# Optimization experiments

Hardware: AMD Instinct MI355X
Metric: run time of the kernel (lower is better)

Reference implementation:

```python
import jax, jax.numpy as jnp
import numpy as np

N_NODES = 100000
IN_CH = 128
HID = 128   # 2 * out_channels
OUT = 64
N_EDGES = 1600000


def gcn_conv(x, W, b, src, dst, n_nodes):
    """PyG GCNConv: add self-loops, symmetric normalization D^-1/2 (A+I) D^-1/2 X W + b."""
    h = x @ W  # [N, F_out]
    ones = jnp.ones(dst.shape[0], dtype=h.dtype)
    # degree of target nodes, +1 for self loop
    deg = jax.ops.segment_sum(ones, dst, num_segments=n_nodes) + 1.0
    dinv = jnp.where(deg > 0, jax.lax.rsqrt(deg), 0.0)  # [N]
    norm = dinv[src] * dinv[dst]  # [E]
    agg = jax.ops.segment_sum(h[src] * norm[:, None], dst, num_segments=n_nodes)
    # self-loop contribution: norm_ii = dinv_i^2 (avoids materializing extra edges)
    agg = agg + h * (dinv * dinv)[:, None]
    return agg + b


def setup_inputs() -> dict:
    key = jax.random.key(0)
    ks = jax.random.split(key, 8)
    x = jax.random.normal(ks[0], (N_NODES, IN_CH), dtype=jnp.float32)
    edge_index = jax.random.randint(ks[1], (2, N_EDGES), 0, N_NODES, dtype=jnp.int64)
    # Glorot-style params
    W1 = jax.random.normal(ks[2], (IN_CH, HID), dtype=jnp.float32) / np.sqrt(IN_CH)
    b1 = jnp.zeros((HID,), dtype=jnp.float32)
    W_mu = jax.random.normal(ks[3], (HID, OUT), dtype=jnp.float32) / np.sqrt(HID)
    b_mu = jnp.zeros((OUT,), dtype=jnp.float32)
    W_ls = jax.random.normal(ks[4], (HID, OUT), dtype=jnp.float32) / np.sqrt(HID)
    b_ls = jnp.zeros((OUT,), dtype=jnp.float32)
    return {"x": x, "edge_index": edge_index, "W1": W1, "b1": b1,
            "W_mu": W_mu, "b_mu": b_mu, "W_ls": W_ls, "b_ls": b_ls}


def reference(x, edge_index, W1, b1, W_mu, b_mu, W_ls, b_ls):
    src, dst = edge_index[0], edge_index[1]
    n = x.shape[0]
    h = jax.nn.relu(gcn_conv(x, W1, b1, src, dst, n))
    mu = gcn_conv(h, W_mu, b_mu, src, dst, n)
    logstd = gcn_conv(h, W_ls, b_ls, src, dst, n)
    return (mu, logstd)
```

## Files before the change

kernel.cpp:

```cpp
#include <hip/hip_runtime.h>
#include <hip/hip_bf16.h>
#include <hip/hip_fp16.h>
#include <stdint.h>

#define N_NODES 100000
#define IN_CH   128
#define HID     128
#define OUT_CH  64
#define N_EDGES 1600000

#define NB    196
#define NBLK  250
#define EPB   6400

typedef __attribute__((ext_vector_type(8))) short  s16x8;
typedef __attribute__((ext_vector_type(4))) float  f32x4;

__device__ __forceinline__ __half2 as_h2(unsigned int u) { return *(__half2*)&u; }


__global__ __launch_bounds__(256) void k_phaseA(const int* __restrict__ dst,
                                                int* __restrict__ Cm) {
    __shared__ int hist[NB];
    int blk = blockIdx.x, t = threadIdx.x;
    if (t < NB) hist[t] = 0;
    __syncthreads();
    int base = blk * EPB;
#pragma unroll 5
    for (int k = 0; k < EPB / 256; k++) {
        int d = dst[base + k * 256 + t];
        atomicAdd(&hist[d >> 9], 1);
    }
    __syncthreads();
    if (t < NB) Cm[blk * NB + t] = hist[t];
}

__global__ __launch_bounds__(256) void k_scanBkt(int* __restrict__ Cm,
                                                 int* __restrict__ bktSum) {
    __shared__ int sdata[256];
    int b = blockIdx.x, t = threadIdx.x;
    int v = (t < NBLK) ? Cm[t * NB + b] : 0;
    sdata[t] = v;
    __syncthreads();
    int val = v;
    for (int off = 1; off < 256; off <<= 1) {
        int tmp = (t >= off) ? sdata[t - off] : 0;
        __syncthreads();
        val += tmp;
        sdata[t] = val;
        __syncthreads();
    }
    if (t < NBLK) Cm[t * NB + b] = val - v;
    if (t == 255) bktSum[b] = val;
}

__global__ __launch_bounds__(256) void k_scanBase(const int* __restrict__ bktSum,
                                                  int* __restrict__ bktBase) {
    __shared__ int sdata[256];
    int t = threadIdx.x;
    int v = (t < NB) ? bktSum[t] : 0;
    sdata[t] = v;
    __syncthreads();
    int val = v;
    for (int off = 1; off < 256; off <<= 1) {
        int tmp = (t >= off) ? sdata[t - off] : 0;
        __syncthreads();
        val += tmp;
        sdata[t] = val;
        __syncthreads();
    }
    if (t < NB) bktBase[t] = val - v;
    if (t == 0) bktBase[NB] = N_EDGES;
}

__global__ __launch_bounds__(256) void k_phaseB(const int* __restrict__ src,
                                                const int* __restrict__ dst,
                                                const int* __restrict__ Cm,
                                                const int* __restrict__ bktBase,
                                                unsigned int* __restrict__ bucketed) {
    __shared__ int offs[NB];
    int blk = blockIdx.x, t = threadIdx.x;
    if (t < NB) offs[t] = Cm[blk * NB + t] + bktBase[t];
    __syncthreads();
    int base = blk * EPB;
#pragma unroll 5
    for (int k = 0; k < EPB / 256; k++) {
        int e = base + k * 256 + t;
        int d = dst[e];
        int sv = src[e];
        int pos = atomicAdd(&offs[d >> 9], 1);
        bucketed[pos] = ((unsigned int)sv << 9) | (unsigned int)(d & 511);
    }
}

__global__ __launch_bounds__(512) void k_phaseC(const unsigned int* __restrict__ bucketed,
                                                const int* __restrict__ bktBase,
                                                int* __restrict__ rowptr,
                                                float* __restrict__ dinvg,
                                                unsigned int* __restrict__ dinvh2,
                                                int* __restrict__ csr_src) {
    __shared__ int cnt[512];
    __shared__ int cur[512];
    __shared__ int sdata[512];
    int b = blockIdx.x, t = threadIdx.x;
    int base = bktBase[b], endR = bktBase[b + 1];
    int nodeBase = b << 9;
    int nNodes = N_NODES - nodeBase;
    if (nNodes > 512) nNodes = 512;

    cnt[t] = 0;
    __syncthreads();
    for (int e = base + t; e < endR; e += 512)
        atomicAdd(&cnt[bucketed[e] & 511], 1);
    __syncthreads();

    int s = cnt[t];
    sdata[t] = s;
    __syncthreads();
    int val = s;
    for (int off = 1; off < 512; off <<= 1) {
        int tmp = (t >= off) ? sdata[t - off] : 0;
        __syncthreads();
        val += tmp;
        sdata[t] = val;
        __syncthreads();
    }
    cur[t] = val - s;
    if (t < nNodes) {
        rowptr[nodeBase + t] = base + val - s;
        float dv = rsqrtf((float)s + 1.0f);
        dinvg[nodeBase + t] = dv;
        __half hd = __float2half(dv);
        unsigned int hu = *(unsigned short*)&hd;
        dinvh2[nodeBase + t] = hu | (hu << 16);
    }
    if (b == NB - 1 && t == 0) rowptr[N_NODES] = N_EDGES;
    __syncthreads();

    for (int e = base + t; e < endR; e += 512) {
        unsigned int u = bucketed[e];
        int pos = base + atomicAdd(&cur[u & 511], 1);
        csr_src[pos] = (int)(u >> 9);
    }
}


__global__ __launch_bounds__(256) void k_prepW(const float* __restrict__ W1,
                                               const float* __restrict__ Wmu,
                                               const float* __restrict__ Wls,
                                               unsigned short* __restrict__ Wt1,
                                               unsigned short* __restrict__ WtC) {
    int idx = blockIdx.x * 256 + threadIdx.x;
    int n = idx >> 7, k = idx & 127;
    __half a = __float2half(W1[k * 128 + n]);
    __half b = __float2half((n < 64) ? Wmu[k * 64 + n] : Wls[k * 64 + (n - 64)]);
    Wt1[idx] = *(unsigned short*)&a;
    WtC[idx] = *(unsigned short*)&b;
}


#define LDA 136

__device__ __forceinline__ void gemm_core(const unsigned short* sA,
                                          const unsigned short* __restrict__ Wt,
                                          unsigned short* __restrict__ Y,
                                          int R0, int t) {
    int wv = t >> 6, l = t & 63;
    int quad = l >> 4, lm = l & 15;

    s16x8 a[2][4];
#pragma unroll
    for (int mt = 0; mt < 2; mt++)
#pragma unroll
        for (int ks = 0; ks < 4; ks++)
            a[mt][ks] = *(const s16x8*)(sA + (wv * 32 + mt * 16 + lm) * LDA +
                                        ks * 32 + quad * 8);

    f32x4 acc[2][8] = {};
#pragma unroll
    for (int nt = 0; nt < 8; nt++) {
        s16x8 b[4];
        const unsigned short* Wp = Wt + (nt * 16 + lm) * 128 + quad * 8;
#pragma unroll
        for (int ks = 0; ks < 4; ks++)
            b[ks] = *(const s16x8*)(Wp + ks * 32);
#pragma unroll
        for (int mt = 0; mt < 2; mt++) {
            f32x4 c = acc[mt][nt];
#pragma unroll
            for (int ks = 0; ks < 4; ks++)
                c = __builtin_amdgcn_mfma_f32_16x16x32_f16(a[mt][ks], b[ks], c, 0, 0, 0);
            acc[mt][nt] = c;
        }
    }

    int rbase = R0 + wv * 32 + quad * 4;
#pragma unroll
    for (int mt = 0; mt < 2; mt++)
#pragma unroll
        for (int nt = 0; nt < 8; nt++)
#pragma unroll
            for (int reg = 0; reg < 4; reg++) {
                int r = rbase + mt * 16 + reg;
                if (r < N_NODES) {
                    __half hv = __float2half(acc[mt][nt][reg]);
                    Y[(size_t)r * 128 + nt * 16 + lm] = *(unsigned short*)&hv;
                }
            }
}

__global__ __launch_bounds__(256) void k_gemm1(const float* __restrict__ X,
                                               const unsigned short* __restrict__ Wt,
                                               unsigned short* __restrict__ Y) {
    __shared__ unsigned short sA[128 * LDA];
    int t = threadIdx.x;
    int R0 = blockIdx.x * 128;
    int row = t >> 1, colb = (t & 1) * 64;
    bool valid = (R0 + row) < N_NODES;
    const float* Xr = X + (size_t)(R0 + row) * 128 + colb;
    unsigned short* dp = sA + row * LDA + colb;
#pragma unroll
    for (int j = 0; j < 16; j++) {
        float4 v = valid ? *(const float4*)(Xr + j * 4) : make_float4(0.f, 0.f, 0.f, 0.f);
        __half2 p0 = __floats2half2_rn(v.x, v.y);
        __half2 p1 = __floats2half2_rn(v.z, v.w);
        uint2 o;
        o.x = *(unsigned int*)&p0;
        o.y = *(unsigned int*)&p1;
        *(uint2*)(dp + j * 4) = o;
    }
    __syncthreads();
    gemm_core(sA, Wt, Y, R0, t);
}

__global__ __launch_bounds__(256) void k_gemm2(const unsigned short* __restrict__ Xh,
                                               const unsigned short* __restrict__ Wt,
                                               unsigned short* __restrict__ Y) {
    __shared__ unsigned short sA[128 * LDA];
    int t = threadIdx.x;
    int R0 = blockIdx.x * 128;
    int row = t >> 1, colb = (t & 1) * 64;
    bool valid = (R0 + row) < N_NODES;
    const unsigned short* Xr = Xh + (size_t)(R0 + row) * 128 + colb;
    unsigned short* dp = sA + row * LDA + colb;
#pragma unroll
    for (int j = 0; j < 8; j++) {
        uint4 v = valid ? *(const uint4*)(Xr + j * 8) : make_uint4(0u, 0u, 0u, 0u);
        *(uint4*)(dp + j * 8) = v;
    }
    __syncthreads();
    gemm_core(sA, Wt, Y, R0, t);
}


__device__ __forceinline__ float2 agg_gather(const unsigned short* __restrict__ tbl,
                                             const int* __restrict__ rowptr,
                                             const int* __restrict__ csr_src,
                                             const unsigned int* __restrict__ dh2,
                                             const float* __restrict__ dinv,
                                             int i, int c2, float* di_out) {
    float di = dinv[i];
    *di_out = di;
    unsigned int sv = *(const unsigned int*)(tbl + (size_t)i * 128 + c2);
    __half2 acc = __floats2half2_rn(0.f, 0.f);
    int beg = rowptr[i], end = rowptr[i + 1];
    for (int p = beg; p < end; p += 8) {
        int s[8]; unsigned int nv[8]; unsigned int r[8];
#pragma unroll
        for (int j = 0; j < 8; j++) {
            int q = p + j;
            s[j] = csr_src[q < end ? q : end - 1];
        }
#pragma unroll
        for (int j = 0; j < 8; j++) nv[j] = dh2[s[j]];
#pragma unroll
        for (int j = 0; j < 8; j++)
            r[j] = *(const unsigned int*)(tbl + (size_t)s[j] * 128 + c2);
#pragma unroll
        for (int j = 0; j < 8; j++) {
            unsigned int nn = (p + j < end) ? nv[j] : 0u;
            acc = __hfma2(as_h2(r[j]), as_h2(nn), acc);
        }
    }
    float2 f = __half22float2(acc);
    float2 hs = __half22float2(as_h2(sv));
    f.x = di * f.x + di * di * hs.x;
    f.y = di * f.y + di * di * hs.y;
    return f;
}

__global__ __launch_bounds__(256) void k_agg1(const unsigned short* __restrict__ h0,
                                              const int* __restrict__ rowptr,
                                              const int* __restrict__ csr_src,
                                              const unsigned int* __restrict__ dh2,
                                              const float* __restrict__ dinv,
                                              const float* __restrict__ b1,
                                              unsigned short* __restrict__ hb) {
    int lane = threadIdx.x & 63;
    int i = __builtin_amdgcn_readfirstlane(blockIdx.x * 4 + (threadIdx.x >> 6));
    int c2 = lane * 2;
    float di;
    float2 f = agg_gather(h0, rowptr, csr_src, dh2, dinv, i, c2, &di);
    f.x += b1[c2];
    f.y += b1[c2 + 1];
    f.x = f.x > 0.f ? f.x : 0.f;
    f.y = f.y > 0.f ? f.y : 0.f;
    __half2 o = __floats2half2_rn(f.x, f.y);
    *(unsigned int*)(hb + (size_t)i * 128 + c2) = *(unsigned int*)&o;
}

__global__ __launch_bounds__(256) void k_agg2(const unsigned short* __restrict__ tt,
                                              const int* __restrict__ rowptr,
                                              const int* __restrict__ csr_src,
                                              const unsigned int* __restrict__ dh2,
                                              const float* __restrict__ dinv,
                                              const float* __restrict__ bmu,
                                              const float* __restrict__ bls,
                                              float* __restrict__ out) {
    int lane = threadIdx.x & 63;
    int i = __builtin_amdgcn_readfirstlane(blockIdx.x * 4 + (threadIdx.x >> 6));
    int c2 = lane * 2;
    float di;
    float2 f = agg_gather(tt, rowptr, csr_src, dh2, dinv, i, c2, &di);
    if (lane < 32) {
        int c = c2;
        *(float2*)(out + (size_t)i * 64 + c) =
            make_float2(f.x + bmu[c], f.y + bmu[c + 1]);
    } else {
        int c = c2 - 64;
        *(float2*)(out + (size_t)N_NODES * 64 + (size_t)i * 64 + c) =
            make_float2(f.x + bls[c], f.y + bls[c + 1]);
    }
}


extern "C" void kernel_launch(void* const* d_in, const int* in_sizes, int n_in,
                              void* d_out, int out_size, void* d_ws, size_t ws_size,
                              hipStream_t stream) {
    const float* x    = (const float*)d_in[0];
    const int*   ei   = (const int*)d_in[1];
    const float* W1   = (const float*)d_in[2];
    const float* b1   = (const float*)d_in[3];
    const float* Wmu  = (const float*)d_in[4];
    const float* bmu  = (const float*)d_in[5];
    const float* Wls  = (const float*)d_in[6];
    const float* bls  = (const float*)d_in[7];
    const int* src = ei;
    const int* dst = ei + N_EDGES;

    char* p = (char*)d_ws;
    unsigned short* bufA = (unsigned short*)p; p += (size_t)N_NODES * 128 * 2;
    unsigned short* bufH = (unsigned short*)p; p += (size_t)N_NODES * 128 * 2;
    unsigned short* Wt1  = (unsigned short*)p; p += 128 * 128 * 2;
    unsigned short* WtC  = (unsigned short*)p; p += 128 * 128 * 2;
    int*   Cm      = (int*)p;   p += (size_t)NBLK * NB * 4;
    int*   bktSum  = (int*)p;   p += 256 * 4;
    int*   bktBase = (int*)p;   p += 256 * 4;
    int*   rowptr  = (int*)p;   p += 400016;
    float* dinv    = (float*)p; p += 400000;
    unsigned int* dinvh2 = (unsigned int*)p; p += 400000;
    unsigned int* bucketed = (unsigned int*)p; p += (size_t)N_EDGES * 4;
    int*   csr_src = (int*)p;   p += (size_t)N_EDGES * 4;

    k_phaseA<<<NBLK, 256, 0, stream>>>(dst, Cm);
    k_scanBkt<<<NB, 256, 0, stream>>>(Cm, bktSum);
    k_scanBase<<<1, 256, 0, stream>>>(bktSum, bktBase);
    k_phaseB<<<NBLK, 256, 0, stream>>>(src, dst, Cm, bktBase, bucketed);
    k_phaseC<<<NB, 512, 0, stream>>>(bucketed, bktBase, rowptr, dinv, dinvh2, csr_src);

    k_prepW<<<64, 256, 0, stream>>>(W1, Wmu, Wls, Wt1, WtC);

    int gblk = (N_NODES + 127) / 128;

    k_gemm1<<<gblk, 256, 0, stream>>>(x, Wt1, bufA);
    k_agg1<<<N_NODES / 4, 256, 0, stream>>>(bufA, rowptr, csr_src, dinvh2, dinv, b1, bufH);

    k_gemm2<<<gblk, 256, 0, stream>>>(bufH, WtC, bufA);
    k_agg2<<<N_NODES / 4, 256, 0, stream>>>(bufA, rowptr, csr_src, dinvh2, dinv,
                                            bmu, bls, (float*)d_out);
}
```

Before: 350.6 us.

## Store feature tables in 16-column slices and gather per slice across edges

The GEMM outputs and the hidden activations move from row-major [N,128] half to eight column slices of [N,16], each slice a contiguous array. Each aggregation block now handles one slice for four nodes. Within a wavefront, 8 lane groups each take a different edge and each lane loads 4 bytes of the slice, and the partial sums are combined with cross-lane shuffles. This keeps every gathered slice table small (about 3.2 MB) so it can stay resident in cache and improve hit rates on the random gathers. The cost is eight times more blocks, each re-reading the CSR indices and normalisation factors once per slice, plus extra shuffle reductions.

```diff
diff --git a/kernel.cpp b/kernel.cpp
--- a/kernel.cpp
+++ b/kernel.cpp
@@ -12,6 +12,8 @@
 #define NB    196
 #define NBLK  250
 #define EPB   6400
+
+#define SS    ((size_t)N_NODES * 16)
 
 typedef __attribute__((ext_vector_type(8))) short  s16x8;
 typedef __attribute__((ext_vector_type(4))) float  f32x4;
@@ -204,7 +206,7 @@
                 int r = rbase + mt * 16 + reg;
                 if (r < N_NODES) {
                     __half hv = __float2half(acc[mt][nt][reg]);
-                    Y[(size_t)r * 128 + nt * 16 + lm] = *(unsigned short*)&hv;
+                    Y[(size_t)nt * SS + (size_t)r * 16 + lm] = *(unsigned short*)&hv;
                 }
             }
 }
@@ -233,54 +235,59 @@
     gemm_core(sA, Wt, Y, R0, t);
 }
 
-__global__ __launch_bounds__(256) void k_gemm2(const unsigned short* __restrict__ Xh,
+__global__ __launch_bounds__(256) void k_gemm2(const unsigned short* __restrict__ Xs,
                                                const unsigned short* __restrict__ Wt,
                                                unsigned short* __restrict__ Y) {
     __shared__ unsigned short sA[128 * LDA];
     int t = threadIdx.x;
     int R0 = blockIdx.x * 128;
-    int row = t >> 1, colb = (t & 1) * 64;
-    bool valid = (R0 + row) < N_NODES;
-    const unsigned short* Xr = Xh + (size_t)(R0 + row) * 128 + colb;
-    unsigned short* dp = sA + row * LDA + colb;
-#pragma unroll
-    for (int j = 0; j < 8; j++) {
-        uint4 v = valid ? *(const uint4*)(Xr + j * 8) : make_uint4(0u, 0u, 0u, 0u);
-        *(uint4*)(dp + j * 8) = v;
+    int q = t >> 5;
+    int sub = t & 31;
+    int part = (sub & 1) * 8;
+#pragma unroll
+    for (int rr = 0; rr < 8; rr++) {
+        int row = rr * 16 + (sub >> 1);
+        int gr = R0 + row;
+        uint4 v = (gr < N_NODES)
+                      ? *(const uint4*)(Xs + (size_t)q * SS + (size_t)gr * 16 + part)
+                      : make_uint4(0u, 0u, 0u, 0u);
+        *(uint4*)(sA + row * LDA + q * 16 + part) = v;
     }
     __syncthreads();
     gemm_core(sA, Wt, Y, R0, t);
 }
 
 
-__device__ __forceinline__ float2 agg_gather(const unsigned short* __restrict__ tbl,
-                                             const int* __restrict__ rowptr,
-                                             const int* __restrict__ csr_src,
-                                             const unsigned int* __restrict__ dh2,
-                                             const float* __restrict__ dinv,
-                                             int i, int c2, float* di_out) {
+__device__ __forceinline__ float2 agg_gather_sl(const unsigned short* __restrict__ tb,
+                                                const int* __restrict__ rowptr,
+                                                const int* __restrict__ csr_src,
+                                                const unsigned int* __restrict__ dh2,
+                                                const float* __restrict__ dinv,
+                                                int i, int l) {
+    int g = l >> 3;
+    int cl = l & 7;
     float di = dinv[i];
-    *di_out = di;
-    unsigned int sv = *(const unsigned int*)(tbl + (size_t)i * 128 + c2);
+    unsigned int sv = *(const unsigned int*)(tb + (size_t)i * 16 + cl * 2);
     __half2 acc = __floats2half2_rn(0.f, 0.f);
     int beg = rowptr[i], end = rowptr[i + 1];
-    for (int p = beg; p < end; p += 8) {
-        int s[8]; unsigned int nv[8]; unsigned int r[8];
-#pragma unroll
-        for (int j = 0; j < 8; j++) {
-            int q = p + j;
-            s[j] = csr_src[q < end ? q : end - 1];
-        }
-#pragma unroll
-        for (int j = 0; j < 8; j++) nv[j] = dh2[s[j]];
-#pragma unroll
-        for (int j = 0; j < 8; j++)
-            r[j] = *(const unsigned int*)(tbl + (size_t)s[j] * 128 + c2);
-#pragma unroll
-        for (int j = 0; j < 8; j++) {
-            unsigned int nn = (p + j < end) ? nv[j] : 0u;
-            acc = __hfma2(as_h2(r[j]), as_h2(nn), acc);
-        }
+    for (int p = beg; p < end; p += 16) {
+        int q0 = p + g, q1 = p + 8 + g;
+        int s0 = __builtin_nontemporal_load(csr_src + (q0 < end ? q0 : end - 1));
+        int s1 = __builtin_nontemporal_load(csr_src + (q1 < end ? q1 : end - 1));
+        unsigned int n0 = dh2[s0];
+        unsigned int n1 = dh2[s1];
+        unsigned int r0 = *(const unsigned int*)(tb + (size_t)s0 * 16 + cl * 2);
+        unsigned int r1 = *(const unsigned int*)(tb + (size_t)s1 * 16 + cl * 2);
+        n0 = (q0 < end) ? n0 : 0u;
+        n1 = (q1 < end) ? n1 : 0u;
+        acc = __hfma2(as_h2(r0), as_h2(n0), acc);
+        acc = __hfma2(as_h2(r1), as_h2(n1), acc);
+    }
+#pragma unroll
+    for (int m = 8; m <= 32; m <<= 1) {
+        int v = *(int*)&acc;
+        int u = __shfl_xor(v, m);
+        acc = __hadd2(acc, *(__half2*)&u);
     }
     float2 f = __half22float2(acc);
     float2 hs = __half22float2(as_h2(sv));
@@ -296,17 +303,22 @@
                                               const float* __restrict__ dinv,
                                               const float* __restrict__ b1,
                                               unsigned short* __restrict__ hb) {
-    int lane = threadIdx.x & 63;
-    int i = __builtin_amdgcn_readfirstlane(blockIdx.x * 4 + (threadIdx.x >> 6));
-    int c2 = lane * 2;
-    float di;
-    float2 f = agg_gather(h0, rowptr, csr_src, dh2, dinv, i, c2, &di);
-    f.x += b1[c2];
-    f.y += b1[c2 + 1];
-    f.x = f.x > 0.f ? f.x : 0.f;
-    f.y = f.y > 0.f ? f.y : 0.f;
-    __half2 o = __floats2half2_rn(f.x, f.y);
-    *(unsigned int*)(hb + (size_t)i * 128 + c2) = *(unsigned int*)&o;
+    int l = threadIdx.x & 63;
+    int wv = threadIdx.x >> 6;
+    int slice = blockIdx.x & 7;
+    int i = __builtin_amdgcn_readfirstlane((blockIdx.x >> 3) * 4 + wv);
+    const unsigned short* tb = h0 + (size_t)slice * SS;
+    float2 f = agg_gather_sl(tb, rowptr, csr_src, dh2, dinv, i, l);
+    if (l < 8) {
+        int c = slice * 16 + l * 2;
+        f.x += b1[c];
+        f.y += b1[c + 1];
+        f.x = f.x > 0.f ? f.x : 0.f;
+        f.y = f.y > 0.f ? f.y : 0.f;
+        __half2 o = __floats2half2_rn(f.x, f.y);
+        *(unsigned int*)(hb + (size_t)slice * SS + (size_t)i * 16 + l * 2) =
+            *(unsigned int*)&o;
+    }
 }
 
 __global__ __launch_bounds__(256) void k_agg2(const unsigned short* __restrict__ tt,
@@ -317,19 +329,20 @@
                                               const float* __restrict__ bmu,
                                               const float* __restrict__ bls,
                                               float* __restrict__ out) {
-    int lane = threadIdx.x & 63;
-    int i = __builtin_amdgcn_readfirstlane(blockIdx.x * 4 + (threadIdx.x >> 6));
-    int c2 = lane * 2;
-    float di;
-    float2 f = agg_gather(tt, rowptr, csr_src, dh2, dinv, i, c2, &di);
-    if (lane < 32) {
-        int c = c2;
-        *(float2*)(out + (size_t)i * 64 + c) =
-            make_float2(f.x + bmu[c], f.y + bmu[c + 1]);
-    } else {
-        int c = c2 - 64;
-        *(float2*)(out + (size_t)N_NODES * 64 + (size_t)i * 64 + c) =
-            make_float2(f.x + bls[c], f.y + bls[c + 1]);
+    int l = threadIdx.x & 63;
+    int wv = threadIdx.x >> 6;
+    int slice = blockIdx.x & 7;
+    int i = __builtin_amdgcn_readfirstlane((blockIdx.x >> 3) * 4 + wv);
+    const unsigned short* tb = tt + (size_t)slice * SS;
+    float2 f = agg_gather_sl(tb, rowptr, csr_src, dh2, dinv, i, l);
+    if (l < 8) {
+        int c = slice * 16 + l * 2;
+        if (c < 64)
+            *(float2*)(out + (size_t)i * 64 + c) =
+                make_float2(f.x + bmu[c], f.y + bmu[c + 1]);
+        else
+            *(float2*)(out + (size_t)N_NODES * 64 + (size_t)i * 64 + (c - 64)) =
+                make_float2(f.x + bls[c - 64], f.y + bls[c - 63]);
     }
 }
 
@@ -371,11 +384,12 @@
     k_prepW<<<64, 256, 0, stream>>>(W1, Wmu, Wls, Wt1, WtC);
 
     int gblk = (N_NODES + 127) / 128;
+    int ablk = (N_NODES / 4) * 8;
 
     k_gemm1<<<gblk, 256, 0, stream>>>(x, Wt1, bufA);
-    k_agg1<<<N_NODES / 4, 256, 0, stream>>>(bufA, rowptr, csr_src, dinvh2, dinv, b1, bufH);
+    k_agg1<<<ablk, 256, 0, stream>>>(bufA, rowptr, csr_src, dinvh2, dinv, b1, bufH);
 
     k_gemm2<<<gblk, 256, 0, stream>>>(bufH, WtC, bufA);
-    k_agg2<<<N_NODES / 4, 256, 0, stream>>>(bufA, rowptr, csr_src, dinvh2, dinv,
-                                            bmu, bls, (float*)d_out);
-}
+    k_agg2<<<ablk, 256, 0, stream>>>(bufA, rowptr, csr_src, dinvh2, dinv,
+                                     bmu, bls, (float*)d_out);
+}
```

New measurement: 702.1 us. 2x slower.

## Fuse CSR build phases and weight prep into one cooperative kernel

Applied to the files above, without the earlier changes.

Merges the histogram, two scans, bucket scatter, per-bucket CSR finalize and weight transpose into one cooperative kernel that uses grid.sync between phases. This removes five kernel launches and their inter-kernel gaps. Bucket totals are now gathered with global atomics after a memset, and every block recomputes the base scan redundantly. Phase C runs with 256 threads handling two nodes each instead of 512, which lowers the parallelism of that stage.

```diff
diff --git a/kernel.cpp b/kernel.cpp
--- a/kernel.cpp
+++ b/kernel.cpp
@@ -1,7 +1,10 @@
 #include <hip/hip_runtime.h>
+#include <hip/hip_cooperative_groups.h>
 #include <hip/hip_bf16.h>
 #include <hip/hip_fp16.h>
 #include <stdint.h>
+
+namespace cg = cooperative_groups;
 
 #define N_NODES 100000
 #define IN_CH   128
@@ -10,7 +13,7 @@
 #define N_EDGES 1600000
 
 #define NB    196
-#define NBLK  250
+#define CSRG  250
 #define EPB   6400
 
 typedef __attribute__((ext_vector_type(8))) short  s16x8;
@@ -19,70 +22,85 @@
 __device__ __forceinline__ __half2 as_h2(unsigned int u) { return *(__half2*)&u; }
 
 
-__global__ __launch_bounds__(256) void k_phaseA(const int* __restrict__ dst,
-                                                int* __restrict__ Cm) {
+__global__ __launch_bounds__(256) void k_csr(
+    const float* __restrict__ W1, const float* __restrict__ Wmu,
+    const float* __restrict__ Wls,
+    unsigned short* __restrict__ Wt1, unsigned short* __restrict__ WtC,
+    const int* __restrict__ src, const int* __restrict__ dst,
+    int* __restrict__ Cm, int* __restrict__ bktSum,
+    unsigned int* __restrict__ bucketed,
+    int* __restrict__ rowptr, float* __restrict__ dinvg,
+    unsigned int* __restrict__ dinvh2, int* __restrict__ csr_src)
+{
+    cg::grid_group grid = cg::this_grid();
     __shared__ int hist[NB];
+    __shared__ int sdata[256];
+    __shared__ int ldsBase[NB + 1];
+    __shared__ int offs[NB];
+    __shared__ int cnt[512];
+    __shared__ int cur2[512];
+
     int blk = blockIdx.x, t = threadIdx.x;
+    int base = blk * EPB;
+
+    int gid = blk * 256 + t;
+    if (gid < 128 * 128) {
+        int n = gid >> 7, k = gid & 127;
+        __half a = __float2half(W1[k * 128 + n]);
+        __half b = __float2half((n < 64) ? Wmu[k * 64 + n] : Wls[k * 64 + (n - 64)]);
+        Wt1[gid] = *(unsigned short*)&a;
+        WtC[gid] = *(unsigned short*)&b;
+    }
+
     if (t < NB) hist[t] = 0;
     __syncthreads();
-    int base = blk * EPB;
 #pragma unroll 5
     for (int k = 0; k < EPB / 256; k++) {
         int d = dst[base + k * 256 + t];
         atomicAdd(&hist[d >> 9], 1);
     }
     __syncthreads();
-    if (t < NB) Cm[blk * NB + t] = hist[t];
-}
-
-__global__ __launch_bounds__(256) void k_scanBkt(int* __restrict__ Cm,
-                                                 int* __restrict__ bktSum) {
-    __shared__ int sdata[256];
-    int b = blockIdx.x, t = threadIdx.x;
-    int v = (t < NBLK) ? Cm[t * NB + b] : 0;
-    sdata[t] = v;
-    __syncthreads();
-    int val = v;
-    for (int off = 1; off < 256; off <<= 1) {
-        int tmp = (t >= off) ? sdata[t - off] : 0;
-        __syncthreads();
-        val += tmp;
-        sdata[t] = val;
-        __syncthreads();
-    }
-    if (t < NBLK) Cm[t * NB + b] = val - v;
-    if (t == 255) bktSum[b] = val;
-}
-
-__global__ __launch_bounds__(256) void k_scanBase(const int* __restrict__ bktSum,
-                                                  int* __restrict__ bktBase) {
-    __shared__ int sdata[256];
-    int t = threadIdx.x;
-    int v = (t < NB) ? bktSum[t] : 0;
-    sdata[t] = v;
-    __syncthreads();
-    int val = v;
-    for (int off = 1; off < 256; off <<= 1) {
-        int tmp = (t >= off) ? sdata[t - off] : 0;
-        __syncthreads();
-        val += tmp;
-        sdata[t] = val;
-        __syncthreads();
-    }
-    if (t < NB) bktBase[t] = val - v;
-    if (t == 0) bktBase[NB] = N_EDGES;
-}
-
-__global__ __launch_bounds__(256) void k_phaseB(const int* __restrict__ src,
-                                                const int* __restrict__ dst,
-                                                const int* __restrict__ Cm,
-                                                const int* __restrict__ bktBase,
-                                                unsigned int* __restrict__ bucketed) {
-    __shared__ int offs[NB];
-    int blk = blockIdx.x, t = threadIdx.x;
-    if (t < NB) offs[t] = Cm[blk * NB + t] + bktBase[t];
-    __syncthreads();
-    int base = blk * EPB;
+    if (t < NB) {
+        int h = hist[t];
+        Cm[blk * NB + t] = h;
+        atomicAdd(&bktSum[t], h);
+    }
+    grid.sync();
+
+    {
+        int v = (blk < NB && t < CSRG) ? Cm[t * NB + blk] : 0;
+        sdata[t] = v;
+        __syncthreads();
+        int val = v;
+        for (int off = 1; off < 256; off <<= 1) {
+            int tmp = (t >= off) ? sdata[t - off] : 0;
+            __syncthreads();
+            val += tmp;
+            sdata[t] = val;
+            __syncthreads();
+        }
+        if (blk < NB && t < CSRG) Cm[t * NB + blk] = val - v;
+    }
+    __syncthreads();
+    {
+        int v = (t < NB) ? bktSum[t] : 0;
+        sdata[t] = v;
+        __syncthreads();
+        int val = v;
+        for (int off = 1; off < 256; off <<= 1) {
+            int tmp = (t >= off) ? sdata[t - off] : 0;
+            __syncthreads();
+            val += tmp;
+            sdata[t] = val;
+            __syncthreads();
+        }
+        if (t < NB) ldsBase[t] = val - v;
+        if (t == 0) ldsBase[NB] = N_EDGES;
+    }
+    grid.sync();
+
+    if (t < NB) offs[t] = Cm[blk * NB + t] + ldsBase[t];
+    __syncthreads();
 #pragma unroll 5
     for (int k = 0; k < EPB / 256; k++) {
         int e = base + k * 256 + t;
@@ -91,71 +109,62 @@
         int pos = atomicAdd(&offs[d >> 9], 1);
         bucketed[pos] = ((unsigned int)sv << 9) | (unsigned int)(d & 511);
     }
-}
-
-__global__ __launch_bounds__(512) void k_phaseC(const unsigned int* __restrict__ bucketed,
-                                                const int* __restrict__ bktBase,
-                                                int* __restrict__ rowptr,
-                                                float* __restrict__ dinvg,
-                                                unsigned int* __restrict__ dinvh2,
-                                                int* __restrict__ csr_src) {
-    __shared__ int cnt[512];
-    __shared__ int cur[512];
-    __shared__ int sdata[512];
-    int b = blockIdx.x, t = threadIdx.x;
-    int base = bktBase[b], endR = bktBase[b + 1];
-    int nodeBase = b << 9;
-    int nNodes = N_NODES - nodeBase;
-    if (nNodes > 512) nNodes = 512;
-
-    cnt[t] = 0;
-    __syncthreads();
-    for (int e = base + t; e < endR; e += 512)
-        atomicAdd(&cnt[bucketed[e] & 511], 1);
-    __syncthreads();
-
-    int s = cnt[t];
-    sdata[t] = s;
-    __syncthreads();
-    int val = s;
-    for (int off = 1; off < 512; off <<= 1) {
-        int tmp = (t >= off) ? sdata[t - off] : 0;
-        __syncthreads();
-        val += tmp;
-        sdata[t] = val;
-        __syncthreads();
-    }
-    cur[t] = val - s;
-    if (t < nNodes) {
-        rowptr[nodeBase + t] = base + val - s;
-        float dv = rsqrtf((float)s + 1.0f);
-        dinvg[nodeBase + t] = dv;
-        __half hd = __float2half(dv);
-        unsigned int hu = *(unsigned short*)&hd;
-        dinvh2[nodeBase + t] = hu | (hu << 16);
-    }
-    if (b == NB - 1 && t == 0) rowptr[N_NODES] = N_EDGES;
-    __syncthreads();
-
-    for (int e = base + t; e < endR; e += 512) {
-        unsigned int u = bucketed[e];
-        int pos = base + atomicAdd(&cur[u & 511], 1);
-        csr_src[pos] = (int)(u >> 9);
-    }
-}
-
-
-__global__ __launch_bounds__(256) void k_prepW(const float* __restrict__ W1,
-                                               const float* __restrict__ Wmu,
-                                               const float* __restrict__ Wls,
-                                               unsigned short* __restrict__ Wt1,
-                                               unsigned short* __restrict__ WtC) {
-    int idx = blockIdx.x * 256 + threadIdx.x;
-    int n = idx >> 7, k = idx & 127;
-    __half a = __float2half(W1[k * 128 + n]);
-    __half b = __float2half((n < 64) ? Wmu[k * 64 + n] : Wls[k * 64 + (n - 64)]);
-    Wt1[idx] = *(unsigned short*)&a;
-    WtC[idx] = *(unsigned short*)&b;
+    grid.sync();
+
+    if (blk < NB) {
+        int b = blk;
+        int base2 = ldsBase[b], endR = ldsBase[b + 1];
+        int nodeBase = b << 9;
+        int nNodes = N_NODES - nodeBase;
+        if (nNodes > 512) nNodes = 512;
+
+        cnt[t] = 0;
+        cnt[t + 256] = 0;
+        __syncthreads();
+        for (int e = base2 + t; e < endR; e += 256)
+            atomicAdd(&cnt[bucketed[e] & 511], 1);
+        __syncthreads();
+
+        int s0 = cnt[2 * t], s1 = cnt[2 * t + 1];
+        int s = s0 + s1;
+        sdata[t] = s;
+        __syncthreads();
+        int val = s;
+        for (int off = 1; off < 256; off <<= 1) {
+            int tmp = (t >= off) ? sdata[t - off] : 0;
+            __syncthreads();
+            val += tmp;
+            sdata[t] = val;
+            __syncthreads();
+        }
+        int excl = val - s;
+        cur2[2 * t] = excl;
+        cur2[2 * t + 1] = excl + s0;
+        if (2 * t < nNodes) {
+            rowptr[nodeBase + 2 * t] = base2 + excl;
+            float dv = rsqrtf((float)s0 + 1.0f);
+            dinvg[nodeBase + 2 * t] = dv;
+            __half hd = __float2half(dv);
+            unsigned int hu = *(unsigned short*)&hd;
+            dinvh2[nodeBase + 2 * t] = hu | (hu << 16);
+        }
+        if (2 * t + 1 < nNodes) {
+            rowptr[nodeBase + 2 * t + 1] = base2 + excl + s0;
+            float dv = rsqrtf((float)s1 + 1.0f);
+            dinvg[nodeBase + 2 * t + 1] = dv;
+            __half hd = __float2half(dv);
+            unsigned int hu = *(unsigned short*)&hd;
+            dinvh2[nodeBase + 2 * t + 1] = hu | (hu << 16);
+        }
+        if (b == NB - 1 && t == 0) rowptr[N_NODES] = N_EDGES;
+        __syncthreads();
+
+        for (int e = base2 + t; e < endR; e += 256) {
+            unsigned int u = bucketed[e];
+            int pos = base2 + atomicAdd(&cur2[u & 511], 1);
+            csr_src[pos] = (int)(u >> 9);
+        }
+    }
 }
 
 
@@ -258,9 +267,8 @@
                                              const int* __restrict__ csr_src,
                                              const unsigned int* __restrict__ dh2,
                                              const float* __restrict__ dinv,
-                                             int i, int c2, float* di_out) {
+                                             int i, int c2) {
     float di = dinv[i];
-    *di_out = di;
     unsigned int sv = *(const unsigned int*)(tbl + (size_t)i * 128 + c2);
     __half2 acc = __floats2half2_rn(0.f, 0.f);
     int beg = rowptr[i], end = rowptr[i + 1];
@@ -299,8 +307,7 @@
     int lane = threadIdx.x & 63;
     int i = __builtin_amdgcn_readfirstlane(blockIdx.x * 4 + (threadIdx.x >> 6));
     int c2 = lane * 2;
-    float di;
-    float2 f = agg_gather(h0, rowptr, csr_src, dh2, dinv, i, c2, &di);
+    float2 f = agg_gather(h0, rowptr, csr_src, dh2, dinv, i, c2);
     f.x += b1[c2];
     f.y += b1[c2 + 1];
     f.x = f.x > 0.f ? f.x : 0.f;
@@ -320,8 +327,7 @@
     int lane = threadIdx.x & 63;
     int i = __builtin_amdgcn_readfirstlane(blockIdx.x * 4 + (threadIdx.x >> 6));
     int c2 = lane * 2;
-    float di;
-    float2 f = agg_gather(tt, rowptr, csr_src, dh2, dinv, i, c2, &di);
+    float2 f = agg_gather(tt, rowptr, csr_src, dh2, dinv, i, c2);
     if (lane < 32) {
         int c = c2;
         *(float2*)(out + (size_t)i * 64 + c) =
@@ -353,22 +359,31 @@
     unsigned short* bufH = (unsigned short*)p; p += (size_t)N_NODES * 128 * 2;
     unsigned short* Wt1  = (unsigned short*)p; p += 128 * 128 * 2;
     unsigned short* WtC  = (unsigned short*)p; p += 128 * 128 * 2;
-    int*   Cm      = (int*)p;   p += (size_t)NBLK * NB * 4;
+    int*   Cm      = (int*)p;   p += (size_t)CSRG * NB * 4;
     int*   bktSum  = (int*)p;   p += 256 * 4;
-    int*   bktBase = (int*)p;   p += 256 * 4;
     int*   rowptr  = (int*)p;   p += 400016;
     float* dinv    = (float*)p; p += 400000;
     unsigned int* dinvh2 = (unsigned int*)p; p += 400000;
     unsigned int* bucketed = (unsigned int*)p; p += (size_t)N_EDGES * 4;
     int*   csr_src = (int*)p;   p += (size_t)N_EDGES * 4;
 
-    k_phaseA<<<NBLK, 256, 0, stream>>>(dst, Cm);
-    k_scanBkt<<<NB, 256, 0, stream>>>(Cm, bktSum);
-    k_scanBase<<<1, 256, 0, stream>>>(bktSum, bktBase);
-    k_phaseB<<<NBLK, 256, 0, stream>>>(src, dst, Cm, bktBase, bucketed);
-    k_phaseC<<<NB, 512, 0, stream>>>(bucketed, bktBase, rowptr, dinv, dinvh2, csr_src);
-
-    k_prepW<<<64, 256, 0, stream>>>(W1, Wmu, Wls, Wt1, WtC);
+    hipMemsetAsync(bktSum, 0, NB * sizeof(int), stream);
+
+    {
+        const float *a0 = W1, *a1 = Wmu, *a2 = Wls;
+        unsigned short *a3 = Wt1, *a4 = WtC;
+        const int *a5 = src, *a6 = dst;
+        int *a7 = Cm, *a8 = bktSum;
+        unsigned int *a9 = bucketed;
+        int *a10 = rowptr;
+        float *a11 = dinv;
+        unsigned int *a12 = dinvh2;
+        int *a13 = csr_src;
+        void* args[] = {&a0, &a1, &a2, &a3, &a4, &a5, &a6, &a7, &a8,
+                        &a9, &a10, &a11, &a12, &a13};
+        hipLaunchCooperativeKernel((const void*)k_csr, dim3(CSRG), dim3(256),
+                                   args, 0, stream);
+    }
 
     int gblk = (N_NODES + 127) / 128;
 
```

Measured after the change: 452.9 us. +29.2%, slower.
